# Kernel tuning notes

Hardware: AMD Instinct MI355X
Metric: run time of the kernel (lower is better)

The kernel has to match this reference:

```python
import jax, jax.numpy as jnp
import numpy as np

FEAT = 1024   # feat_dim
EMB = 64      # emb_dim
GROUP = 16    # group == fc_dim
DG = FEAT // GROUP  # 64, per-group query/key dim and conv out channels per group
R = 1024      # num_rois
N = 1024      # nongt_dim


def setup_inputs() -> dict:
    key = jax.random.key(0)
    ks = jax.random.split(key, 8)
    inp = {
        "position_embedding": jax.random.normal(ks[0], (R, N, EMB), dtype=jnp.float32),
        "roi_feat": jax.random.normal(ks[1], (R, FEAT), dtype=jnp.float32),
        # fc_q / fc_k: Linear(feat_dim, feat_dim)
        "Wq": jax.random.normal(ks[2], (FEAT, FEAT), dtype=jnp.float32) * 0.02,
        "bq": jnp.zeros((FEAT,), dtype=jnp.float32),
        "Wk": jax.random.normal(ks[3], (FEAT, FEAT), dtype=jnp.float32) * 0.02,
        "bk": jnp.zeros((FEAT,), dtype=jnp.float32),
        # fc_pos_feat: Linear(emb_dim, fc_dim=group)
        "Wp": jax.random.normal(ks[4], (GROUP, EMB), dtype=jnp.float32) * 0.1,
        "bp": jnp.zeros((GROUP,), dtype=jnp.float32),
        # conv_cat: Conv2d(group*feat_dim, feat_dim, k=1, groups=group)
        # per group g: in FEAT channels -> out DG channels. Shape [GROUP, DG, FEAT].
        "Wc": jax.random.normal(ks[5], (GROUP, DG, FEAT), dtype=jnp.float32) * 0.02,
        "bc": jnp.zeros((FEAT,), dtype=jnp.float32),
        "nongt_dim": N,
    }
    return inp


def reference(position_embedding, roi_feat, Wq, bq, Wk, bk, Wp, bp, Wc, bc, nongt_dim):
    scale = 1.0 / np.sqrt(float(DG))
    # fc_pos_feat + relu -> aff_weight [R, GROUP, N]
    pos_feat = jax.nn.relu(jnp.einsum("rne,ge->rng", position_embedding, Wp) + bp)
    aff_weight = jnp.transpose(pos_feat, (0, 2, 1))  # [R, GROUP, N]
    nongt = roi_feat[:nongt_dim]                     # [N, FEAT]
    q = (roi_feat @ Wq.T + bq).reshape(-1, GROUP, DG)   # [R, GROUP, DG]
    k = (nongt @ Wk.T + bk).reshape(-1, GROUP, DG)      # [N, GROUP, DG]
    # per-group QK^T with log position bias
    aff = jnp.einsum("rgd,ngd->rgn", q, k) * scale      # [R, GROUP, N]
    weighted = jnp.log(jnp.clip(aff_weight, 1e-6, None)) + aff
    att = jax.nn.softmax(weighted, axis=2)              # [R, GROUP, N]
    # attention * V -> [R, GROUP, FEAT]
    out_t = jnp.einsum("rgn,nf->rgf", att, nongt)
    # grouped 1x1 conv combine: group g maps FEAT -> DG output channels
    out = jnp.einsum("rgf,gof->rgo", out_t, Wc).reshape(-1, FEAT) + bc
    return out
```

## Files before the change

### kernel.cpp

```cpp
#include <hip/hip_runtime.h>

#define R_DIM 1024
#define N_DIM 1024
#define FEAT  1024
#define EMB   64
#define GROUP 16
#define DG    64

typedef _Float16 half8  __attribute__((ext_vector_type(8)));
typedef _Float16 half4v __attribute__((ext_vector_type(4)));
typedef float    f32x4  __attribute__((ext_vector_type(4)));

__device__ __forceinline__ half8 cvt8(const float* p) {
  const float4 a = *(const float4*)p;
  const float4 b = *(const float4*)(p + 4);
  half8 h;
  h[0] = (_Float16)a.x; h[1] = (_Float16)a.y; h[2] = (_Float16)a.z; h[3] = (_Float16)a.w;
  h[4] = (_Float16)b.x; h[5] = (_Float16)b.y; h[6] = (_Float16)b.z; h[7] = (_Float16)b.w;
  return h;
}
__device__ __forceinline__ half8 cvt8x(f32x4 a, f32x4 b) {
  half8 h;
  h[0] = (_Float16)a[0]; h[1] = (_Float16)a[1]; h[2] = (_Float16)a[2]; h[3] = (_Float16)a[3];
  h[4] = (_Float16)b[0]; h[5] = (_Float16)b[1]; h[6] = (_Float16)b[2]; h[7] = (_Float16)b[3];
  return h;
}
__device__ __forceinline__ f32x4 ntld(const float* p) {
  return __builtin_nontemporal_load((const f32x4*)p);
}

__global__ __launch_bounds__(256) void qk_gemm(
    const float* __restrict__ roi, const float* __restrict__ Wq,
    const float* __restrict__ bq,  const float* __restrict__ Wk,
    const float* __restrict__ bk,  _Float16* __restrict__ qhI,
    _Float16* __restrict__ khI)
{
  __shared__ float aT[16][68];
  __shared__ float bqT[16][68];
  __shared__ float bkT[16][68];
  const int t  = threadIdx.x;
  const int r0 = blockIdx.x * 64, c0 = blockIdx.y * 64;
  const int lr = t >> 2, lk = (t & 3) << 2;
  const int ty = t >> 4, tx = t & 15;
  const float* ap  = roi + (r0 + lr) * FEAT + lk;
  const float* bqp = Wq  + (c0 + lr) * FEAT + lk;
  const float* bkp = Wk  + (c0 + lr) * FEAT + lk;
  float4 av  = *(const float4*)ap;
  float4 bqv = *(const float4*)bqp;
  float4 bkv = *(const float4*)bkp;
  float accq[4][4] = {}, acck[4][4] = {};
  for (int k0 = 0; k0 < FEAT; k0 += 16) {
    aT[lk+0][lr]=av.x;   aT[lk+1][lr]=av.y;   aT[lk+2][lr]=av.z;   aT[lk+3][lr]=av.w;
    bqT[lk+0][lr]=bqv.x; bqT[lk+1][lr]=bqv.y; bqT[lk+2][lr]=bqv.z; bqT[lk+3][lr]=bqv.w;
    bkT[lk+0][lr]=bkv.x; bkT[lk+1][lr]=bkv.y; bkT[lk+2][lr]=bkv.z; bkT[lk+3][lr]=bkv.w;
    __syncthreads();
    const bool more = (k0 + 16) < FEAT;
    float4 av_n, bqv_n, bkv_n;
    if (more) {
      av_n  = *(const float4*)(ap  + k0 + 16);
      bqv_n = *(const float4*)(bqp + k0 + 16);
      bkv_n = *(const float4*)(bkp + k0 + 16);
    }
#pragma unroll
    for (int kk = 0; kk < 16; ++kk) {
      const float4 a4 = *(const float4*)&aT[kk][ty << 2];
      const float4 q4 = *(const float4*)&bqT[kk][tx << 2];
      const float4 k4 = *(const float4*)&bkT[kk][tx << 2];
      const float ar[4] = {a4.x, a4.y, a4.z, a4.w};
      const float qr[4] = {q4.x, q4.y, q4.z, q4.w};
      const float kr[4] = {k4.x, k4.y, k4.z, k4.w};
#pragma unroll
      for (int i = 0; i < 4; ++i)
#pragma unroll
        for (int j = 0; j < 4; ++j) {
          accq[i][j] += ar[i] * qr[j];
          acck[i][j] += ar[i] * kr[j];
        }
    }
    __syncthreads();
    if (more) { av = av_n; bqv = bqv_n; bkv = bkv_n; }
  }
  const float4 bq4 = *(const float4*)(bq + c0 + (tx << 2));
  const float4 bk4 = *(const float4*)(bk + c0 + (tx << 2));
  const float bqr[4] = {bq4.x, bq4.y, bq4.z, bq4.w};
  const float bkr[4] = {bk4.x, bk4.y, bk4.z, bk4.w};
  const int g = c0 >> 6;
#pragma unroll
  for (int i = 0; i < 4; ++i) {
    half4v oq, ok;
#pragma unroll
    for (int j = 0; j < 4; ++j) {
      oq[j] = (_Float16)(accq[i][j] + bqr[j]);
      ok[j] = (_Float16)(acck[i][j] + bkr[j]);
    }
    const int row = r0 + (ty << 2) + i;
    const size_t idx = ((((size_t)g << 3) + (tx >> 1)) << 13) + ((size_t)row << 3) + ((tx & 1) << 2);
    *(half4v*)(qhI + idx) = oq;
    *(half4v*)(khI + idx) = ok;
  }
}

__global__ __launch_bounds__(256) void pos_mfma(
    const float* __restrict__ pe, const float* __restrict__ Wp,
    const float* __restrict__ bp, _Float16* __restrict__ logw)
{
  const int t = threadIdx.x;
  const int w = t >> 6, l = t & 63, q16 = l & 15, q4 = l >> 4;
  const float* wpp = Wp + (q16 << 6) + (q4 << 3);
  const half8 wb0 = cvt8(wpp);
  const half8 wb1 = cvt8(wpp + 32);
  const float bpg = bp[q16];

  const int tile0 = ((blockIdx.x << 2) + w) << 2;
  const float* src = pe + ((size_t)tile0 << 10) + (q16 << 6) + (q4 << 3);

  f32x4 c0 = ntld(src);
  f32x4 c1 = ntld(src + 4);
  f32x4 c2 = ntld(src + 32);
  f32x4 c3 = ntld(src + 36);
#pragma unroll
  for (int it = 0; it < 4; ++it) {
    f32x4 n0, n1, n2, n3;
    if (it < 3) {
      const float* s2 = src + ((size_t)(it + 1) << 10);
      n0 = ntld(s2);
      n1 = ntld(s2 + 4);
      n2 = ntld(s2 + 32);
      n3 = ntld(s2 + 36);
    }
    __builtin_amdgcn_sched_barrier(0);
    const half8 a0 = cvt8x(c0, c1);
    const half8 a1 = cvt8x(c2, c3);
    f32x4 acc = (f32x4){0.f, 0.f, 0.f, 0.f};
    acc = __builtin_amdgcn_mfma_f32_16x16x32_f16(a0, wb0, acc, 0, 0, 0);
    acc = __builtin_amdgcn_mfma_f32_16x16x32_f16(a1, wb1, acc, 0, 0, 0);
    half4v o;
#pragma unroll
    for (int j = 0; j < 4; ++j)
      o[j] = (_Float16)__logf(fmaxf(acc[j] + bpg, 1e-6f));
    const int tt = tile0 + it;
    const int r  = tt >> 6;
    const int nb = ((tt & 63) << 4) + (q4 << 2);
    *(half4v*)(logw + ((((size_t)r << 4) + q16) << 10) + nb) = o;
    if (it < 3) { c0 = n0; c1 = n1; c2 = n2; c3 = n3; }
  }
}

__global__ __launch_bounds__(256) void kc_gemm(
    const float* __restrict__ roi, const float* __restrict__ Wc,
    _Float16* __restrict__ kctI)
{
  __shared__ float aT[16][68];
  __shared__ float bT[16][68];
  const int t   = threadIdx.x;
  const int n0g = blockIdx.x * 64;
  const int g   = blockIdx.y;
  const int lr = t >> 2, lk = (t & 3) << 2;
  const int ty = t >> 4, tx = t & 15;
  const float* ap  = Wc  + (size_t)(g * DG + lr) * FEAT + lk;
  const float* bp_ = roi + (size_t)(n0g + lr) * FEAT + lk;
  float4 av = *(const float4*)ap;
  float4 bv = *(const float4*)bp_;
  float acc[4][4] = {};
  for (int k0 = 0; k0 < FEAT; k0 += 16) {
    aT[lk+0][lr]=av.x; aT[lk+1][lr]=av.y; aT[lk+2][lr]=av.z; aT[lk+3][lr]=av.w;
    bT[lk+0][lr]=bv.x; bT[lk+1][lr]=bv.y; bT[lk+2][lr]=bv.z; bT[lk+3][lr]=bv.w;
    __syncthreads();
    const bool more = (k0 + 16) < FEAT;
    float4 av_n, bv_n;
    if (more) {
      av_n = *(const float4*)(ap  + k0 + 16);
      bv_n = *(const float4*)(bp_ + k0 + 16);
    }
#pragma unroll
    for (int kk = 0; kk < 16; ++kk) {
      const float4 a4 = *(const float4*)&aT[kk][ty << 2];
      const float4 b4 = *(const float4*)&bT[kk][tx << 2];
      const float ar[4] = {a4.x, a4.y, a4.z, a4.w};
      const float br[4] = {b4.x, b4.y, b4.z, b4.w};
#pragma unroll
      for (int i = 0; i < 4; ++i)
#pragma unroll
        for (int j = 0; j < 4; ++j) acc[i][j] += ar[i] * br[j];
    }
    __syncthreads();
    if (more) { av = av_n; bv = bv_n; }
  }
#pragma unroll
  for (int i = 0; i < 4; ++i) {
    half4v o4;
#pragma unroll
    for (int j = 0; j < 4; ++j) o4[j] = (_Float16)acc[i][j];
    *(half4v*)(kctI + ((((size_t)g << 7) + ((n0g + (tx << 2)) >> 3)) << 9)
               + (((ty << 2) + i) << 3) + ((tx & 1) << 2)) = o4;
  }
}

#define PLD 1032
__global__ __launch_bounds__(256) void attn_mfma(
    const _Float16* __restrict__ qhI, const _Float16* __restrict__ khI,
    const _Float16* __restrict__ logw, const _Float16* __restrict__ kctI,
    const float* __restrict__ bc, float* __restrict__ outp)
{
  __shared__ __align__(16) union ShMem {
    _Float16 P[16][PLD];
    float    Ored[4][16][68];
  } sh;
  __shared__ float redm[4][16];
  __shared__ float redl[4][16];

  const int t   = threadIdx.x;
  const int w   = t >> 6;
  const int l   = t & 63;
  const int q16 = l & 15;
  const int q4  = l >> 4;
  const int g   = blockIdx.y;
  const int r0  = blockIdx.x << 4;
  const int nbase = w << 8;

  const _Float16* kbase = khI  + ((size_t)g << 16);
  const _Float16* qbase = qhI  + ((size_t)g << 16);
  const _Float16* cbase = kctI + ((size_t)g << 16);

  const half8 b0 = *(const half8*)(qbase + ((size_t)q4 << 13) + ((r0 + q16) << 3));
  const half8 b1 = *(const half8*)(qbase + ((size_t)(4 + q4) << 13) + ((r0 + q16) << 3));

  f32x4 S[16];
#pragma unroll
  for (int i = 0; i < 16; ++i) S[i] = (f32x4){0.f, 0.f, 0.f, 0.f};
#pragma unroll
  for (int t16 = 0; t16 < 16; ++t16) {
    const int n = nbase + (t16 << 4) + q16;
    const half8 k0 = *(const half8*)(kbase + ((size_t)q4 << 13) + (n << 3));
    const half8 k1 = *(const half8*)(kbase + ((size_t)(4 + q4) << 13) + (n << 3));
    S[t16] = __builtin_amdgcn_mfma_f32_16x16x32_f16(k0, b0, S[t16], 0, 0, 0);
    S[t16] = __builtin_amdgcn_mfma_f32_16x16x32_f16(k1, b1, S[t16], 0, 0, 0);
  }
  const _Float16* lwp = logw + ((((size_t)(r0 + q16)) << 4) + (size_t)g) * 1024;
#pragma unroll
  for (int t16 = 0; t16 < 16; ++t16) {
    const half4v lw = *(const half4v*)(lwp + nbase + (t16 << 4) + (q4 << 2));
#pragma unroll
    for (int j = 0; j < 4; ++j)
      S[t16][j] = S[t16][j] * 0.125f + (float)lw[j];
  }

  float m = -1e30f;
#pragma unroll
  for (int t16 = 0; t16 < 16; ++t16)
#pragma unroll
    for (int j = 0; j < 4; ++j) m = fmaxf(m, S[t16][j]);
  m = fmaxf(m, __shfl_xor(m, 16));
  m = fmaxf(m, __shfl_xor(m, 32));
  if (q4 == 0) redm[w][q16] = m;
  __syncthreads();
  m = fmaxf(fmaxf(redm[0][q16], redm[1][q16]), fmaxf(redm[2][q16], redm[3][q16]));

  float ls = 0.f;
#pragma unroll
  for (int t16 = 0; t16 < 16; ++t16) {
    half4v pv;
#pragma unroll
    for (int j = 0; j < 4; ++j) {
      const float p = __expf(S[t16][j] - m);
      ls += p;
      pv[j] = (_Float16)p;
    }
    *(half4v*)&sh.P[q16][nbase + (t16 << 4) + (q4 << 2)] = pv;
  }
  ls += __shfl_xor(ls, 16);
  ls += __shfl_xor(ls, 32);
  if (q4 == 0) redl[w][q16] = ls;
  __syncthreads();

  f32x4 O[4];
#pragma unroll
  for (int ot = 0; ot < 4; ++ot) O[ot] = (f32x4){0.f, 0.f, 0.f, 0.f};
#pragma unroll
  for (int ks = 0; ks < 8; ++ks) {
    const int nk = nbase + (ks << 5) + (q4 << 3);
    const half8 pa = *(const half8*)&sh.P[q16][nk];
#pragma unroll
    for (int ot = 0; ot < 4; ++ot) {
      const half8 bfr = *(const half8*)(cbase + ((size_t)(nk >> 3) << 9) + (((ot << 4) + q16) << 3));
      O[ot] = __builtin_amdgcn_mfma_f32_16x16x32_f16(pa, bfr, O[ot], 0, 0, 0);
    }
  }
  __syncthreads();
#pragma unroll
  for (int ot = 0; ot < 4; ++ot)
#pragma unroll
    for (int j = 0; j < 4; ++j)
      sh.Ored[w][(q4 << 2) + j][(ot << 4) + q16] = O[ot][j];
  __syncthreads();

  const int r  = t >> 4;
  const int o0 = (t & 15) << 2;
  const float lsum = redl[0][r] + redl[1][r] + redl[2][r] + redl[3][r];
  const float inv  = 1.0f / lsum;
  float o[4];
#pragma unroll
  for (int c = 0; c < 4; ++c)
    o[c] = sh.Ored[0][r][o0 + c] + sh.Ored[1][r][o0 + c] + sh.Ored[2][r][o0 + c] + sh.Ored[3][r][o0 + c];
  const float4 bcv = *(const float4*)(bc + (g << 6) + o0);
  float4 res;
  res.x = o[0] * inv + bcv.x;
  res.y = o[1] * inv + bcv.y;
  res.z = o[2] * inv + bcv.z;
  res.w = o[3] * inv + bcv.w;
  *(float4*)(outp + (size_t)(r0 + r) * FEAT + (g << 6) + o0) = res;
}

extern "C" void kernel_launch(void* const* d_in, const int* in_sizes, int n_in,
                              void* d_out, int out_size, void* d_ws, size_t ws_size,
                              hipStream_t stream)
{
  const float* pe  = (const float*)d_in[0];
  const float* roi = (const float*)d_in[1];
  const float* Wq  = (const float*)d_in[2];
  const float* bq  = (const float*)d_in[3];
  const float* Wk  = (const float*)d_in[4];
  const float* bk  = (const float*)d_in[5];
  const float* Wp  = (const float*)d_in[6];
  const float* bp  = (const float*)d_in[7];
  const float* Wc  = (const float*)d_in[8];
  const float* bc  = (const float*)d_in[9];
  float* outp = (float*)d_out;

  char* ws = (char*)d_ws;
  _Float16* qhI  = (_Float16*)(ws);
  _Float16* khI  = (_Float16*)(ws + ((size_t)2 << 20));
  _Float16* kctI = (_Float16*)(ws + ((size_t)4 << 20));
  _Float16* logw = (_Float16*)(ws + ((size_t)6 << 20));

  qk_gemm<<<dim3(16, 16), 256, 0, stream>>>(roi, Wq, bq, Wk, bk, qhI, khI);
  pos_mfma<<<4096, 256, 0, stream>>>(pe, Wp, bp, logw);
  kc_gemm<<<dim3(16, 16), 256, 0, stream>>>(roi, Wc, kctI);
  attn_mfma<<<dim3(64, 16), 256, 0, stream>>>(qhI, khI, logw, kctI, bc, outp);
}
```

Baseline: 202.4 us.

## Fuse all stages into one persistent kernel with atomic work queue and flags

Replaces the four separate launches with a single 1024-block kernel. Blocks pull producer work items (QK gemm, KC gemm, position log-weights) from an atomic counter, then each block runs one attention tile after spinning on per-row readiness counters. The aim is to remove launch gaps and let attention on early rows overlap with position-embedding processing on later rows. It adds a memset, atomics and spin-waits that depend on all blocks being co-resident, and it drops the nontemporal loads on position_embedding.

```diff
diff --git a/kernel.cpp b/kernel.cpp
--- a/kernel.cpp
+++ b/kernel.cpp
@@ -6,6 +6,7 @@
 #define EMB   64
 #define GROUP 16
 #define DG    64
+#define PLD   1032
 
 typedef _Float16 half8  __attribute__((ext_vector_type(8)));
 typedef _Float16 half4v __attribute__((ext_vector_type(4)));
@@ -25,21 +26,21 @@
   h[4] = (_Float16)b[0]; h[5] = (_Float16)b[1]; h[6] = (_Float16)b[2]; h[7] = (_Float16)b[3];
   return h;
 }
-__device__ __forceinline__ f32x4 ntld(const float* p) {
-  return __builtin_nontemporal_load((const f32x4*)p);
-}
-
-__global__ __launch_bounds__(256) void qk_gemm(
-    const float* __restrict__ roi, const float* __restrict__ Wq,
-    const float* __restrict__ bq,  const float* __restrict__ Wk,
-    const float* __restrict__ bk,  _Float16* __restrict__ qhI,
-    _Float16* __restrict__ khI)
-{
-  __shared__ float aT[16][68];
-  __shared__ float bqT[16][68];
-  __shared__ float bkT[16][68];
+
+union ShMem {
+  struct { float aT[16][68]; float b0T[16][68]; float b1T[16][68]; } gm;
+  _Float16 P[16][PLD];
+  float    Ored[4][16][68];
+};
+
+__device__ __forceinline__ void qk_item(
+    int k, const float* __restrict__ roi, const float* __restrict__ Wq,
+    const float* __restrict__ bq, const float* __restrict__ Wk,
+    const float* __restrict__ bk, _Float16* __restrict__ qhI,
+    _Float16* __restrict__ khI, ShMem& sh)
+{
   const int t  = threadIdx.x;
-  const int r0 = blockIdx.x * 64, c0 = blockIdx.y * 64;
+  const int r0 = (k >> 4) << 6, c0 = (k & 15) << 6;
   const int lr = t >> 2, lk = (t & 3) << 2;
   const int ty = t >> 4, tx = t & 15;
   const float* ap  = roi + (r0 + lr) * FEAT + lk;
@@ -50,9 +51,9 @@
   float4 bkv = *(const float4*)bkp;
   float accq[4][4] = {}, acck[4][4] = {};
   for (int k0 = 0; k0 < FEAT; k0 += 16) {
-    aT[lk+0][lr]=av.x;   aT[lk+1][lr]=av.y;   aT[lk+2][lr]=av.z;   aT[lk+3][lr]=av.w;
-    bqT[lk+0][lr]=bqv.x; bqT[lk+1][lr]=bqv.y; bqT[lk+2][lr]=bqv.z; bqT[lk+3][lr]=bqv.w;
-    bkT[lk+0][lr]=bkv.x; bkT[lk+1][lr]=bkv.y; bkT[lk+2][lr]=bkv.z; bkT[lk+3][lr]=bkv.w;
+    sh.gm.aT [lk+0][lr]=av.x;  sh.gm.aT [lk+1][lr]=av.y;  sh.gm.aT [lk+2][lr]=av.z;  sh.gm.aT [lk+3][lr]=av.w;
+    sh.gm.b0T[lk+0][lr]=bqv.x; sh.gm.b0T[lk+1][lr]=bqv.y; sh.gm.b0T[lk+2][lr]=bqv.z; sh.gm.b0T[lk+3][lr]=bqv.w;
+    sh.gm.b1T[lk+0][lr]=bkv.x; sh.gm.b1T[lk+1][lr]=bkv.y; sh.gm.b1T[lk+2][lr]=bkv.z; sh.gm.b1T[lk+3][lr]=bkv.w;
     __syncthreads();
     const bool more = (k0 + 16) < FEAT;
     float4 av_n, bqv_n, bkv_n;
@@ -63,9 +64,9 @@
     }
 #pragma unroll
     for (int kk = 0; kk < 16; ++kk) {
-      const float4 a4 = *(const float4*)&aT[kk][ty << 2];
-      const float4 q4 = *(const float4*)&bqT[kk][tx << 2];
-      const float4 k4 = *(const float4*)&bkT[kk][tx << 2];
+      const float4 a4 = *(const float4*)&sh.gm.aT [kk][ty << 2];
+      const float4 q4 = *(const float4*)&sh.gm.b0T[kk][tx << 2];
+      const float4 k4 = *(const float4*)&sh.gm.b1T[kk][tx << 2];
       const float ar[4] = {a4.x, a4.y, a4.z, a4.w};
       const float qr[4] = {q4.x, q4.y, q4.z, q4.w};
       const float kr[4] = {k4.x, k4.y, k4.z, k4.w};
@@ -100,61 +101,13 @@
   }
 }
 
-__global__ __launch_bounds__(256) void pos_mfma(
-    const float* __restrict__ pe, const float* __restrict__ Wp,
-    const float* __restrict__ bp, _Float16* __restrict__ logw)
-{
-  const int t = threadIdx.x;
-  const int w = t >> 6, l = t & 63, q16 = l & 15, q4 = l >> 4;
-  const float* wpp = Wp + (q16 << 6) + (q4 << 3);
-  const half8 wb0 = cvt8(wpp);
-  const half8 wb1 = cvt8(wpp + 32);
-  const float bpg = bp[q16];
-
-  const int tile0 = ((blockIdx.x << 2) + w) << 2;
-  const float* src = pe + ((size_t)tile0 << 10) + (q16 << 6) + (q4 << 3);
-
-  f32x4 c0 = ntld(src);
-  f32x4 c1 = ntld(src + 4);
-  f32x4 c2 = ntld(src + 32);
-  f32x4 c3 = ntld(src + 36);
-#pragma unroll
-  for (int it = 0; it < 4; ++it) {
-    f32x4 n0, n1, n2, n3;
-    if (it < 3) {
-      const float* s2 = src + ((size_t)(it + 1) << 10);
-      n0 = ntld(s2);
-      n1 = ntld(s2 + 4);
-      n2 = ntld(s2 + 32);
-      n3 = ntld(s2 + 36);
-    }
-    __builtin_amdgcn_sched_barrier(0);
-    const half8 a0 = cvt8x(c0, c1);
-    const half8 a1 = cvt8x(c2, c3);
-    f32x4 acc = (f32x4){0.f, 0.f, 0.f, 0.f};
-    acc = __builtin_amdgcn_mfma_f32_16x16x32_f16(a0, wb0, acc, 0, 0, 0);
-    acc = __builtin_amdgcn_mfma_f32_16x16x32_f16(a1, wb1, acc, 0, 0, 0);
-    half4v o;
-#pragma unroll
-    for (int j = 0; j < 4; ++j)
-      o[j] = (_Float16)__logf(fmaxf(acc[j] + bpg, 1e-6f));
-    const int tt = tile0 + it;
-    const int r  = tt >> 6;
-    const int nb = ((tt & 63) << 4) + (q4 << 2);
-    *(half4v*)(logw + ((((size_t)r << 4) + q16) << 10) + nb) = o;
-    if (it < 3) { c0 = n0; c1 = n1; c2 = n2; c3 = n3; }
-  }
-}
-
-__global__ __launch_bounds__(256) void kc_gemm(
-    const float* __restrict__ roi, const float* __restrict__ Wc,
-    _Float16* __restrict__ kctI)
-{
-  __shared__ float aT[16][68];
-  __shared__ float bT[16][68];
+__device__ __forceinline__ void kc_item(
+    int k, const float* __restrict__ roi, const float* __restrict__ Wc,
+    _Float16* __restrict__ kctI, ShMem& sh)
+{
   const int t   = threadIdx.x;
-  const int n0g = blockIdx.x * 64;
-  const int g   = blockIdx.y;
+  const int g   = k >> 4;
+  const int n0g = (k & 15) << 6;
   const int lr = t >> 2, lk = (t & 3) << 2;
   const int ty = t >> 4, tx = t & 15;
   const float* ap  = Wc  + (size_t)(g * DG + lr) * FEAT + lk;
@@ -163,8 +116,8 @@
   float4 bv = *(const float4*)bp_;
   float acc[4][4] = {};
   for (int k0 = 0; k0 < FEAT; k0 += 16) {
-    aT[lk+0][lr]=av.x; aT[lk+1][lr]=av.y; aT[lk+2][lr]=av.z; aT[lk+3][lr]=av.w;
-    bT[lk+0][lr]=bv.x; bT[lk+1][lr]=bv.y; bT[lk+2][lr]=bv.z; bT[lk+3][lr]=bv.w;
+    sh.gm.aT [lk+0][lr]=av.x; sh.gm.aT [lk+1][lr]=av.y; sh.gm.aT [lk+2][lr]=av.z; sh.gm.aT [lk+3][lr]=av.w;
+    sh.gm.b0T[lk+0][lr]=bv.x; sh.gm.b0T[lk+1][lr]=bv.y; sh.gm.b0T[lk+2][lr]=bv.z; sh.gm.b0T[lk+3][lr]=bv.w;
     __syncthreads();
     const bool more = (k0 + 16) < FEAT;
     float4 av_n, bv_n;
@@ -174,8 +127,8 @@
     }
 #pragma unroll
     for (int kk = 0; kk < 16; ++kk) {
-      const float4 a4 = *(const float4*)&aT[kk][ty << 2];
-      const float4 b4 = *(const float4*)&bT[kk][tx << 2];
+      const float4 a4 = *(const float4*)&sh.gm.aT [kk][ty << 2];
+      const float4 b4 = *(const float4*)&sh.gm.b0T[kk][tx << 2];
       const float ar[4] = {a4.x, a4.y, a4.z, a4.w};
       const float br[4] = {b4.x, b4.y, b4.z, b4.w};
 #pragma unroll
@@ -196,26 +149,104 @@
   }
 }
 
-#define PLD 1032
-__global__ __launch_bounds__(256) void attn_mfma(
-    const _Float16* __restrict__ qhI, const _Float16* __restrict__ khI,
-    const _Float16* __restrict__ logw, const _Float16* __restrict__ kctI,
-    const float* __restrict__ bc, float* __restrict__ outp)
-{
-  __shared__ __align__(16) union ShMem {
-    _Float16 P[16][PLD];
-    float    Ored[4][16][68];
-  } sh;
+__device__ __forceinline__ void pos_item(
+    int p, const float* __restrict__ pe, const float* __restrict__ Wp,
+    const float* __restrict__ bp, _Float16* __restrict__ logw)
+{
+  const int t = threadIdx.x;
+  const int w = t >> 6, l = t & 63, q16 = l & 15, q4 = l >> 4;
+  const float* wpp = Wp + (q16 << 6) + (q4 << 3);
+  const half8 wb0 = cvt8(wpp);
+  const half8 wb1 = cvt8(wpp + 32);
+  const float bpg = bp[q16];
+
+  const float* s0 = pe + ((size_t)p << 16) + (w << 14) + (q16 << 6) + (q4 << 3);
+  f32x4 c0 = *(const f32x4*)(s0);
+  f32x4 c1 = *(const f32x4*)(s0 + 4);
+  f32x4 c2 = *(const f32x4*)(s0 + 32);
+  f32x4 c3 = *(const f32x4*)(s0 + 36);
+#pragma unroll
+  for (int it = 0; it < 16; ++it) {
+    f32x4 n0, n1, n2, n3;
+    if (it < 15) {
+      const float* s2 = s0 + ((size_t)(it + 1) << 10);
+      n0 = *(const f32x4*)(s2);
+      n1 = *(const f32x4*)(s2 + 4);
+      n2 = *(const f32x4*)(s2 + 32);
+      n3 = *(const f32x4*)(s2 + 36);
+    }
+    __builtin_amdgcn_sched_barrier(0);
+    const half8 a0 = cvt8x(c0, c1);
+    const half8 a1 = cvt8x(c2, c3);
+    f32x4 acc = (f32x4){0.f, 0.f, 0.f, 0.f};
+    acc = __builtin_amdgcn_mfma_f32_16x16x32_f16(a0, wb0, acc, 0, 0, 0);
+    acc = __builtin_amdgcn_mfma_f32_16x16x32_f16(a1, wb1, acc, 0, 0, 0);
+    half4v o;
+#pragma unroll
+    for (int j = 0; j < 4; ++j)
+      o[j] = (_Float16)__logf(fmaxf(acc[j] + bpg, 1e-6f));
+    const int nb = (((w << 4) + it) << 4) + (q4 << 2);
+    *(half4v*)(logw + ((((size_t)p << 4) + q16) << 10) + nb) = o;
+    if (it < 15) { c0 = n0; c1 = n1; c2 = n2; c3 = n3; }
+  }
+}
+
+__global__ __launch_bounds__(256) void fused(
+    const float* __restrict__ pe,  const float* __restrict__ roi,
+    const float* __restrict__ Wq,  const float* __restrict__ bq,
+    const float* __restrict__ Wk,  const float* __restrict__ bk,
+    const float* __restrict__ Wp,  const float* __restrict__ bp,
+    const float* __restrict__ Wc,  const float* __restrict__ bc,
+    _Float16* __restrict__ qhI, _Float16* __restrict__ khI,
+    _Float16* __restrict__ kctI, _Float16* __restrict__ logw,
+    float* __restrict__ outp, unsigned* __restrict__ sync)
+{
+  __shared__ ShMem sh;
   __shared__ float redm[4][16];
   __shared__ float redl[4][16];
-
-  const int t   = threadIdx.x;
+  __shared__ unsigned sh_item;
+
+  const int t = threadIdx.x;
+
+  for (;;) {
+    if (t == 0)
+      sh_item = __hip_atomic_fetch_add(&sync[0], 1u, __ATOMIC_RELAXED, __HIP_MEMORY_SCOPE_AGENT);
+    __syncthreads();
+    const unsigned k = sh_item;
+    if (k >= 1536u) break;
+    if (k < 256u)       qk_item((int)k, roi, Wq, bq, Wk, bk, qhI, khI, sh);
+    else if (k < 512u)  kc_item((int)(k - 256u), roi, Wc, kctI, sh);
+    else                pos_item((int)(k - 512u), pe, Wp, bp, logw);
+    __threadfence();
+    __syncthreads();
+    if (t == 0) {
+      unsigned* ctr = (k < 256u) ? &sync[1]
+                    : (k < 512u) ? &sync[2]
+                                 : &sync[16 + ((k - 512u) >> 4)];
+      __hip_atomic_fetch_add(ctr, 1u, __ATOMIC_RELEASE, __HIP_MEMORY_SCOPE_AGENT);
+    }
+    __syncthreads();
+  }
+
+  const int bid = blockIdx.x;
+  const int i   = bid >> 4;
+  const int g   = bid & 15;
+  if (t == 0) {
+    while (__hip_atomic_load(&sync[1], __ATOMIC_ACQUIRE, __HIP_MEMORY_SCOPE_AGENT) < 256u)
+      __builtin_amdgcn_s_sleep(2);
+    while (__hip_atomic_load(&sync[2], __ATOMIC_ACQUIRE, __HIP_MEMORY_SCOPE_AGENT) < 256u)
+      __builtin_amdgcn_s_sleep(2);
+    while (__hip_atomic_load(&sync[16 + i], __ATOMIC_ACQUIRE, __HIP_MEMORY_SCOPE_AGENT) < 16u)
+      __builtin_amdgcn_s_sleep(2);
+  }
+  __syncthreads();
+  __threadfence();
+
   const int w   = t >> 6;
   const int l   = t & 63;
   const int q16 = l & 15;
   const int q4  = l >> 4;
-  const int g   = blockIdx.y;
-  const int r0  = blockIdx.x << 4;
+  const int r0  = i << 4;
   const int nbase = w << 8;
 
   const _Float16* kbase = khI  + ((size_t)g << 16);
@@ -227,7 +258,7 @@
 
   f32x4 S[16];
 #pragma unroll
-  for (int i = 0; i < 16; ++i) S[i] = (f32x4){0.f, 0.f, 0.f, 0.f};
+  for (int x = 0; x < 16; ++x) S[x] = (f32x4){0.f, 0.f, 0.f, 0.f};
 #pragma unroll
   for (int t16 = 0; t16 < 16; ++t16) {
     const int n = nbase + (t16 << 4) + q16;
@@ -332,9 +363,9 @@
   _Float16* khI  = (_Float16*)(ws + ((size_t)2 << 20));
   _Float16* kctI = (_Float16*)(ws + ((size_t)4 << 20));
   _Float16* logw = (_Float16*)(ws + ((size_t)6 << 20));
-
-  qk_gemm<<<dim3(16, 16), 256, 0, stream>>>(roi, Wq, bq, Wk, bk, qhI, khI);
-  pos_mfma<<<4096, 256, 0, stream>>>(pe, Wp, bp, logw);
-  kc_gemm<<<dim3(16, 16), 256, 0, stream>>>(roi, Wc, kctI);
-  attn_mfma<<<dim3(64, 16), 256, 0, stream>>>(qhI, khI, logw, kctI, bc, outp);
-}
+  unsigned* syncp = (unsigned*)(ws + ((size_t)38 << 20));
+
+  hipMemsetAsync((void*)syncp, 0, 512, stream);
+  fused<<<1024, 256, 0, stream>>>(pe, roi, Wq, bq, Wk, bk, Wp, bp, Wc, bc,
+                                  qhI, khI, kctI, logw, outp, syncp);
+}
```

After: 710.7 us. 251% more time.
